# Kernel optimization log

Hardware: AMD Instinct MI355X
Metric: run time of the kernel (lower is better)

Reference implementation:

```python
import jax, jax.numpy as jnp
import numpy as np

N_NODES = 50000


def gcn_conv(x, src, dst, W, b, n_nodes):
    """PyG GCNConv: add self-loops, sym-normalize, aggregate, linear.
    x' = D^{-1/2} (A + I) D^{-1/2} X W + b
    """
    loop = jnp.arange(n_nodes, dtype=src.dtype)
    s = jnp.concatenate([src, loop])  # [E + N]
    d = jnp.concatenate([dst, loop])
    h = x @ W  # [N, out]
    deg = jax.ops.segment_sum(jnp.ones_like(d, dtype=h.dtype), d, num_segments=n_nodes)
    dinv = jnp.where(deg > 0, jax.lax.rsqrt(deg), 0.0)
    norm = dinv[s] * dinv[d]  # [E + N]
    msg = h[s] * norm[:, None]  # gather + scale (edge-level, memory bound)
    out = jax.ops.segment_sum(msg, d, num_segments=n_nodes)
    return out + b


def setup_inputs() -> dict:
    key = jax.random.key(0)
    k1, k2, k3, k4 = jax.random.split(key, 4)
    n, e, d_in, d_hid, d_out = N_NODES, 800000, 128, 128, 64
    x = jax.random.normal(k1, (n, d_in), dtype=jnp.float32)
    edge_index = jax.random.randint(k2, (2, e), 0, n, dtype=jnp.int64)
    W1 = jax.random.normal(k3, (d_in, d_hid), dtype=jnp.float32) * (1.0 / np.sqrt(d_in))
    b1 = jnp.zeros((d_hid,), dtype=jnp.float32)
    W2 = jax.random.normal(k4, (d_hid, d_out), dtype=jnp.float32) * (1.0 / np.sqrt(d_hid))
    b2 = jnp.zeros((d_out,), dtype=jnp.float32)
    return {"x": x, "edge_index": edge_index, "W1": W1, "b1": b1, "W2": W2, "b2": b2}


def reference(x, edge_index, W1, b1, W2, b2):
    src, dst = edge_index[0], edge_index[1]
    h = gcn_conv(x, src, dst, W1, b1, N_NODES)
    h = jax.nn.relu(h)
    h = gcn_conv(h, src, dst, W2, b2, N_NODES)
    # edge-wise gather + dot product -> per-edge logits [E]
    logits = jnp.sum(h[src] * h[dst], axis=-1)
    return logits
```

## Files before the change

### kernel.cpp

```cpp
#include <hip/hip_runtime.h>
#include <hip/hip_bf16.h>


__global__ void cnt_rank_k(const int* __restrict__ dst, int* __restrict__ cnt,
                           int* __restrict__ rank, int E) {
    int t = blockIdx.x * blockDim.x + threadIdx.x;
    int e = t * 4;
    if (e + 4 <= E) {
        int4 d4 = *reinterpret_cast<const int4*>(dst + e);
        int4 r4;
        r4.x = atomicAdd(&cnt[d4.x], 1);
        r4.y = atomicAdd(&cnt[d4.y], 1);
        r4.z = atomicAdd(&cnt[d4.z], 1);
        r4.w = atomicAdd(&cnt[d4.w], 1);
        *reinterpret_cast<int4*>(rank + e) = r4;
    } else {
        for (int i = e; i < E; i++) rank[i] = atomicAdd(&cnt[dst[i]], 1);
    }
}

__global__ void scan1_k(const int* __restrict__ cnt, int* __restrict__ incl,
                        int* __restrict__ bsum, int N) {
    __shared__ int sh[256];
    int i = blockIdx.x * 256 + threadIdx.x;
    int v = (i < N) ? cnt[i] : 0;
    sh[threadIdx.x] = v;
    __syncthreads();
#pragma unroll
    for (int off = 1; off < 256; off <<= 1) {
        int t = (threadIdx.x >= off) ? sh[threadIdx.x - off] : 0;
        __syncthreads();
        sh[threadIdx.x] += t;
        __syncthreads();
    }
    if (i < N) incl[i] = sh[threadIdx.x];
    if (threadIdx.x == 255) bsum[blockIdx.x] = sh[255];
}

__global__ __launch_bounds__(256) void scan23_k(const int* __restrict__ cnt,
                                                const int* __restrict__ incl,
                                                const int* __restrict__ bsum,
                                                int* __restrict__ rowptr,
                                                float* __restrict__ dinv,
                                                int N, int E, int NB) {
    __shared__ int sh[256];
    __shared__ int blockOff;
    int v = (threadIdx.x < NB) ? bsum[threadIdx.x] : 0;
    sh[threadIdx.x] = v;
    __syncthreads();
#pragma unroll
    for (int off = 1; off < 256; off <<= 1) {
        int t = (threadIdx.x >= off) ? sh[threadIdx.x - off] : 0;
        __syncthreads();
        sh[threadIdx.x] += t;
        __syncthreads();
    }
    if (threadIdx.x == blockIdx.x) blockOff = sh[threadIdx.x] - v;
    __syncthreads();
    int i = blockIdx.x * 256 + threadIdx.x;
    if (i < N) {
        int c = cnt[i];
        rowptr[i] = incl[i] - c + blockOff;
        dinv[i] = rsqrtf(1.0f + (float)c);
    }
    if (i == 0) rowptr[N] = E;
}

template <int BN, bool RELU>
__device__ __forceinline__ void gemm_body32(const float* __restrict__ A,
                                            const float* __restrict__ W,
                                            const float* __restrict__ dscale,
                                            float4* __restrict__ OutT,
                                            int M, int Nn, int row0,
                                            float (*As)[36], float (*Bs)[BN]) {
    constexpr int K = 128, BK = 16;
    constexpr int TN = BN / 16;
    const int tid = threadIdx.x;
    const int tx = tid & 15, ty = tid >> 4;

    float acc[2][TN];
#pragma unroll
    for (int m = 0; m < 2; m++)
#pragma unroll
        for (int n = 0; n < TN; n++) acc[m][n] = 0.0f;

    for (int kt = 0; kt < K; kt += BK) {
        if (tid < 128) {
            int r = tid >> 2;
            int kq = (tid & 3) * 4;
            float4 av = make_float4(0.f, 0.f, 0.f, 0.f);
            int gr = row0 + r;
            if (gr < M)
                av = *reinterpret_cast<const float4*>(A + (size_t)gr * K + kt + kq);
            if (RELU) {
                av.x = fmaxf(av.x, 0.f); av.y = fmaxf(av.y, 0.f);
                av.z = fmaxf(av.z, 0.f); av.w = fmaxf(av.w, 0.f);
            }
            As[kq + 0][r] = av.x; As[kq + 1][r] = av.y;
            As[kq + 2][r] = av.z; As[kq + 3][r] = av.w;
        }
#pragma unroll
        for (int s = 0; s < (BK * BN) / (256 * 4); s++) {
            int f = s * 256 + tid;
            int brow = f / (BN / 4);
            int bcol = (f % (BN / 4)) * 4;
            float4 bv = *reinterpret_cast<const float4*>(W + (size_t)(kt + brow) * BN + bcol);
            *reinterpret_cast<float4*>(&Bs[brow][bcol]) = bv;
        }
        __syncthreads();

#pragma unroll
        for (int k = 0; k < BK; k++) {
            float2 a2 = *reinterpret_cast<const float2*>(&As[k][ty * 2]);
            float a[2] = {a2.x, a2.y};
            float b[TN];
            float4 b0 = *reinterpret_cast<const float4*>(&Bs[k][tx * 4]);
            b[0] = b0.x; b[1] = b0.y; b[2] = b0.z; b[3] = b0.w;
            if (TN == 8) {
                float4 b1 = *reinterpret_cast<const float4*>(&Bs[k][64 + tx * 4]);
                b[4] = b1.x; b[5] = b1.y; b[6] = b1.z; b[7] = b1.w;
            }
#pragma unroll
            for (int m = 0; m < 2; m++)
#pragma unroll
                for (int n = 0; n < TN; n++) acc[m][n] = fmaf(a[m], b[n], acc[m][n]);
        }
        __syncthreads();
    }

    const int chunk0 = tx >> 2;
    const int off = tx & 3;
#pragma unroll
    for (int m = 0; m < 2; m++) {
        int gr = row0 + ty * 2 + m;
        if (gr < M) {
            float dv = dscale[gr];
            float4 o0 = make_float4(acc[m][0] * dv, acc[m][1] * dv,
                                    acc[m][2] * dv, acc[m][3] * dv);
            OutT[((size_t)chunk0 * Nn + gr) * 4 + off] = o0;
            if (TN == 8) {
                float4 o1 = make_float4(acc[m][4] * dv, acc[m][5] * dv,
                                        acc[m][6] * dv, acc[m][7] * dv);
                OutT[((size_t)(4 + chunk0) * Nn + gr) * 4 + off] = o1;
            }
        }
    }
}

__global__ __launch_bounds__(256) void gemm1_fill_k(const float* __restrict__ A,
                                                    const float* __restrict__ W,
                                                    const float* __restrict__ dscale,
                                                    float4* __restrict__ OutT,
                                                    int M, int Nn,
                                                    const int* __restrict__ src,
                                                    const int* __restrict__ dst,
                                                    const int* __restrict__ rowptr,
                                                    const int* __restrict__ rank,
                                                    int* __restrict__ col,
                                                    int* __restrict__ eid, int E,
                                                    int gemmBlocks) {
    __shared__ float As[16][36];
    __shared__ float Bs[16][128];
    int g = (int)blockIdx.x;
    if (g >= gemmBlocks) {
        int t = (g - gemmBlocks) * 256 + threadIdx.x;
        int e = t * 4;
        if (e + 4 <= E) {
            int4 s4 = *reinterpret_cast<const int4*>(src + e);
            int4 d4 = *reinterpret_cast<const int4*>(dst + e);
            int4 r4 = *reinterpret_cast<const int4*>(rank + e);
            int p0 = rowptr[d4.x] + r4.x; col[p0] = s4.x; eid[p0] = e + 0;
            int p1 = rowptr[d4.y] + r4.y; col[p1] = s4.y; eid[p1] = e + 1;
            int p2 = rowptr[d4.z] + r4.z; col[p2] = s4.z; eid[p2] = e + 2;
            int p3 = rowptr[d4.w] + r4.w; col[p3] = s4.w; eid[p3] = e + 3;
        } else {
            for (int i = e; i < E; i++) {
                int pos = rowptr[dst[i]] + rank[i];
                col[pos] = src[i]; eid[pos] = i;
            }
        }
        return;
    }
    gemm_body32<128, false>(A, W, dscale, OutT, M, Nn, g * 32, As, Bs);
}

__global__ __launch_bounds__(256) void gemm2_k(const float* __restrict__ A,
                                               const float* __restrict__ W,
                                               const float* __restrict__ dscale,
                                               float4* __restrict__ OutT,
                                               int M, int Nn) {
    __shared__ float As[16][36];
    __shared__ float Bs[16][64];
    gemm_body32<64, true>(A, W, dscale, OutT, M, Nn, (int)blockIdx.x * 32, As, Bs);
}

__global__ __launch_bounds__(256) void pull128c_k(const int* __restrict__ rowptr,
                                                  const int* __restrict__ col,
                                                  const float4* __restrict__ hsT,
                                                  const float* __restrict__ dinv,
                                                  const float4* __restrict__ bias4,
                                                  float4* __restrict__ out4, int N) {
    int c = (int)(blockIdx.x & 7);
    int g = (int)(blockIdx.x >> 3);
    int v = g * 64 + (int)(threadIdx.x >> 2);
    if (v >= N) return;
    int j = threadIdx.x & 3;
    int p0 = rowptr[v], p1 = rowptr[v + 1];
    size_t cb = (size_t)c * N;

    float4 acc = hsT[(cb + v) * 4 + j];
    int p = p0;
    for (; p + 4 <= p1; p += 4) {
        int u0 = col[p], u1 = col[p + 1], u2 = col[p + 2], u3 = col[p + 3];
        float4 a = hsT[(cb + u0) * 4 + j];
        float4 b = hsT[(cb + u1) * 4 + j];
        float4 cc = hsT[(cb + u2) * 4 + j];
        float4 d = hsT[(cb + u3) * 4 + j];
        acc.x += (a.x + b.x) + (cc.x + d.x);
        acc.y += (a.y + b.y) + (cc.y + d.y);
        acc.z += (a.z + b.z) + (cc.z + d.z);
        acc.w += (a.w + b.w) + (cc.w + d.w);
    }
    for (; p < p1; p++) {
        float4 a = hsT[(cb + col[p]) * 4 + j];
        acc.x += a.x; acc.y += a.y; acc.z += a.z; acc.w += a.w;
    }

    float dv = dinv[v];
    float4 bv = bias4[c * 4 + j];
    out4[(size_t)v * 32 + c * 4 + j] =
        make_float4(fmaf(acc.x, dv, bv.x), fmaf(acc.y, dv, bv.y),
                    fmaf(acc.z, dv, bv.z), fmaf(acc.w, dv, bv.w));
}

__global__ __launch_bounds__(256) void pull64c_k(const int* __restrict__ rowptr,
                                                 const int* __restrict__ col,
                                                 const float4* __restrict__ g2T,
                                                 const float* __restrict__ dinv,
                                                 const float4* __restrict__ bias4,
                                                 float4* __restrict__ out4, int N) {
    int c = (int)(blockIdx.x & 3);
    int g = (int)(blockIdx.x >> 2);
    int v = g * 64 + (int)(threadIdx.x >> 2);
    if (v >= N) return;
    int j = threadIdx.x & 3;
    int p0 = rowptr[v], p1 = rowptr[v + 1];
    size_t cb = (size_t)c * N;

    float4 acc = g2T[(cb + v) * 4 + j];
    int p = p0;
    for (; p + 4 <= p1; p += 4) {
        int u0 = col[p], u1 = col[p + 1], u2 = col[p + 2], u3 = col[p + 3];
        float4 a = g2T[(cb + u0) * 4 + j];
        float4 b = g2T[(cb + u1) * 4 + j];
        float4 cc = g2T[(cb + u2) * 4 + j];
        float4 d = g2T[(cb + u3) * 4 + j];
        acc.x += (a.x + b.x) + (cc.x + d.x);
        acc.y += (a.y + b.y) + (cc.y + d.y);
        acc.z += (a.z + b.z) + (cc.z + d.z);
        acc.w += (a.w + b.w) + (cc.w + d.w);
    }
    for (; p < p1; p++) {
        float4 a = g2T[(cb + col[p]) * 4 + j];
        acc.x += a.x; acc.y += a.y; acc.z += a.z; acc.w += a.w;
    }

    float dv = dinv[v];
    float4 bv = bias4[c * 4 + j];
    out4[(size_t)v * 16 + c * 4 + j] =
        make_float4(fmaf(acc.x, dv, bv.x), fmaf(acc.y, dv, bv.y),
                    fmaf(acc.z, dv, bv.z), fmaf(acc.w, dv, bv.w));
}

__global__ __launch_bounds__(256) void logits_csr_k(const int* __restrict__ rowptr,
                                                    const int* __restrict__ col,
                                                    const int* __restrict__ eid,
                                                    const float4* __restrict__ h4,
                                                    float* __restrict__ out, int N) {
    int v = (int)((blockIdx.x * (size_t)blockDim.x + threadIdx.x) >> 6);
    if (v >= N) return;
    int lane = threadIdx.x & 63;
    int q = lane & 15, slot = lane >> 4;
    int p0 = rowptr[v], p1 = rowptr[v + 1];
    if (p0 == p1) return;

    float4 rd = h4[(size_t)v * 16 + q];

    int p = p0;
    for (; p + 8 <= p1; p += 8) {
        int s0 = col[p + slot], s1 = col[p + 4 + slot];
        int e0 = eid[p + slot], e1 = eid[p + 4 + slot];
        float4 ra = h4[(size_t)s0 * 16 + q];
        float4 rb = h4[(size_t)s1 * 16 + q];
        float t0 = rd.x * ra.x + rd.y * ra.y + rd.z * ra.z + rd.w * ra.w;
        float t1 = rd.x * rb.x + rd.y * rb.y + rd.z * rb.z + rd.w * rb.w;
#pragma unroll
        for (int off = 1; off < 16; off <<= 1) {
            t0 += __shfl_xor(t0, off);
            t1 += __shfl_xor(t1, off);
        }
        if (q == 0) { out[e0] = t0; out[e1] = t1; }
    }
    for (; p + 4 <= p1; p += 4) {
        int s0 = col[p + slot];
        int e0 = eid[p + slot];
        float4 ra = h4[(size_t)s0 * 16 + q];
        float t0 = rd.x * ra.x + rd.y * ra.y + rd.z * ra.z + rd.w * ra.w;
#pragma unroll
        for (int off = 1; off < 16; off <<= 1) t0 += __shfl_xor(t0, off);
        if (q == 0) out[e0] = t0;
    }
    int rem = p1 - p;
    if (slot < rem) {
        int s0 = col[p + slot];
        int e0 = eid[p + slot];
        float4 ra = h4[(size_t)s0 * 16 + q];
        float t0 = rd.x * ra.x + rd.y * ra.y + rd.z * ra.z + rd.w * ra.w;
#pragma unroll
        for (int off = 1; off < 16; off <<= 1) t0 += __shfl_xor(t0, off);
        if (q == 0) out[e0] = t0;
    }
}

extern "C" void kernel_launch(void* const* d_in, const int* in_sizes, int n_in,
                              void* d_out, int out_size, void* d_ws, size_t ws_size,
                              hipStream_t stream) {
    const float* x  = (const float*)d_in[0];
    const int* ei   = (const int*)d_in[1];
    const float* W1 = (const float*)d_in[2];
    const float* b1 = (const float*)d_in[3];
    const float* W2 = (const float*)d_in[4];
    const float* b2 = (const float*)d_in[5];
    float* out = (float*)d_out;

    const int N = in_sizes[0] / 128;
    const int E = in_sizes[1] / 2;
    const int* src = ei;
    const int* dst = ei + E;

    float* ws   = (float*)d_ws;
    float* dinv = ws;
    float* bufA = ws + 50176;
    float* bufB = bufA + (size_t)N * 128;
    float* hsT  = bufA;
    float* agg1 = bufB;
    float* g2T  = bufA;
    float* agg2 = bufA + (size_t)N * 64;

    int* ibase  = (int*)(bufB + (size_t)N * 128);
    int* cnt    = ibase;
    int* incl   = cnt + N;
    int* rowptr = incl + N;
    int* bsum   = rowptr + (N + 1);
    int* rank   = bsum + 256;
    int* col    = rank + E;
    int* eid    = col + E;

    const int B = 256;
    const int NB = (N + 255) / 256;
    const unsigned nodeBlocks = (unsigned)(((size_t)N * 64 + 255) / 256);
    const unsigned ng64 = (unsigned)((N + 63) / 64);

    hipMemsetAsync(cnt, 0, (size_t)N * sizeof(int), stream);
    cnt_rank_k<<<(E / 4 + B - 1) / B, B, 0, stream>>>(dst, cnt, rank, E);
    scan1_k<<<NB, 256, 0, stream>>>(cnt, incl, bsum, N);
    scan23_k<<<NB, 256, 0, stream>>>(cnt, incl, bsum, rowptr, dinv, N, E, NB);

    {
        int gemmBlocks = (N + 31) / 32;
        int fillBlocks = (E / 4 + B - 1) / B;
        gemm1_fill_k<<<gemmBlocks + fillBlocks, 256, 0, stream>>>(
            x, W1, dinv, (float4*)hsT, N, N, src, dst, rowptr, rank, col, eid, E,
            gemmBlocks);
    }

    pull128c_k<<<ng64 * 8, 256, 0, stream>>>(rowptr, col, (const float4*)hsT, dinv,
                                             (const float4*)b1, (float4*)agg1, N);

    gemm2_k<<<(N + 31) / 32, 256, 0, stream>>>(agg1, W2, dinv, (float4*)g2T, N, N);

    pull64c_k<<<ng64 * 4, 256, 0, stream>>>(rowptr, col, (const float4*)g2T, dinv,
                                            (const float4*)b2, (float4*)agg2, N);

    logits_csr_k<<<nodeBlocks, 256, 0, stream>>>(rowptr, col, eid, (const float4*)agg2, out, N);
}
```

Baseline: 232.0 us.

## Compute edge logits in edge order from chunked layout with partial-sum reduction

Drops the eid permutation array and the CSR-ordered logits kernel. The second aggregation now writes its output in the chunk-transposed layout. Logits are computed directly in edge order: each of four column chunks writes a partial dot product per edge, and a second kernel sums the four partials with coalesced float4 loads. This removes the eid scatter writes and the scattered output stores, at the cost of an extra kernel, a 4×E partial buffer, and reading src and dst rows without the CSR locality.

```diff
diff --git a/kernel.cpp b/kernel.cpp
--- a/kernel.cpp
+++ b/kernel.cpp
@@ -156,8 +156,7 @@
                                                     const int* __restrict__ dst,
                                                     const int* __restrict__ rowptr,
                                                     const int* __restrict__ rank,
-                                                    int* __restrict__ col,
-                                                    int* __restrict__ eid, int E,
+                                                    int* __restrict__ col, int E,
                                                     int gemmBlocks) {
     __shared__ float As[16][36];
     __shared__ float Bs[16][128];
@@ -169,15 +168,13 @@
             int4 s4 = *reinterpret_cast<const int4*>(src + e);
             int4 d4 = *reinterpret_cast<const int4*>(dst + e);
             int4 r4 = *reinterpret_cast<const int4*>(rank + e);
-            int p0 = rowptr[d4.x] + r4.x; col[p0] = s4.x; eid[p0] = e + 0;
-            int p1 = rowptr[d4.y] + r4.y; col[p1] = s4.y; eid[p1] = e + 1;
-            int p2 = rowptr[d4.z] + r4.z; col[p2] = s4.z; eid[p2] = e + 2;
-            int p3 = rowptr[d4.w] + r4.w; col[p3] = s4.w; eid[p3] = e + 3;
+            col[rowptr[d4.x] + r4.x] = s4.x;
+            col[rowptr[d4.y] + r4.y] = s4.y;
+            col[rowptr[d4.z] + r4.z] = s4.z;
+            col[rowptr[d4.w] + r4.w] = s4.w;
         } else {
-            for (int i = e; i < E; i++) {
-                int pos = rowptr[dst[i]] + rank[i];
-                col[pos] = src[i]; eid[pos] = i;
-            }
+            for (int i = e; i < E; i++)
+                col[rowptr[dst[i]] + rank[i]] = src[i];
         }
         return;
     }
@@ -238,7 +235,7 @@
                                                  const float4* __restrict__ g2T,
                                                  const float* __restrict__ dinv,
                                                  const float4* __restrict__ bias4,
-                                                 float4* __restrict__ out4, int N) {
+                                                 float4* __restrict__ outT, int N) {
     int c = (int)(blockIdx.x & 3);
     int g = (int)(blockIdx.x >> 2);
     int v = g * 64 + (int)(threadIdx.x >> 2);
@@ -267,58 +264,58 @@
 
     float dv = dinv[v];
     float4 bv = bias4[c * 4 + j];
-    out4[(size_t)v * 16 + c * 4 + j] =
+    outT[(cb + v) * 4 + j] =
         make_float4(fmaf(acc.x, dv, bv.x), fmaf(acc.y, dv, bv.y),
                     fmaf(acc.z, dv, bv.z), fmaf(acc.w, dv, bv.w));
 }
 
-__global__ __launch_bounds__(256) void logits_csr_k(const int* __restrict__ rowptr,
-                                                    const int* __restrict__ col,
-                                                    const int* __restrict__ eid,
-                                                    const float4* __restrict__ h4,
-                                                    float* __restrict__ out, int N) {
-    int v = (int)((blockIdx.x * (size_t)blockDim.x + threadIdx.x) >> 6);
-    if (v >= N) return;
-    int lane = threadIdx.x & 63;
-    int q = lane & 15, slot = lane >> 4;
-    int p0 = rowptr[v], p1 = rowptr[v + 1];
-    if (p0 == p1) return;
-
-    float4 rd = h4[(size_t)v * 16 + q];
-
-    int p = p0;
-    for (; p + 8 <= p1; p += 8) {
-        int s0 = col[p + slot], s1 = col[p + 4 + slot];
-        int e0 = eid[p + slot], e1 = eid[p + 4 + slot];
-        float4 ra = h4[(size_t)s0 * 16 + q];
-        float4 rb = h4[(size_t)s1 * 16 + q];
-        float t0 = rd.x * ra.x + rd.y * ra.y + rd.z * ra.z + rd.w * ra.w;
-        float t1 = rd.x * rb.x + rd.y * rb.y + rd.z * rb.z + rd.w * rb.w;
-#pragma unroll
-        for (int off = 1; off < 16; off <<= 1) {
-            t0 += __shfl_xor(t0, off);
-            t1 += __shfl_xor(t1, off);
-        }
-        if (q == 0) { out[e0] = t0; out[e1] = t1; }
-    }
-    for (; p + 4 <= p1; p += 4) {
-        int s0 = col[p + slot];
-        int e0 = eid[p + slot];
-        float4 ra = h4[(size_t)s0 * 16 + q];
-        float t0 = rd.x * ra.x + rd.y * ra.y + rd.z * ra.z + rd.w * ra.w;
-#pragma unroll
-        for (int off = 1; off < 16; off <<= 1) t0 += __shfl_xor(t0, off);
-        if (q == 0) out[e0] = t0;
-    }
-    int rem = p1 - p;
-    if (slot < rem) {
-        int s0 = col[p + slot];
-        int e0 = eid[p + slot];
-        float4 ra = h4[(size_t)s0 * 16 + q];
-        float t0 = rd.x * ra.x + rd.y * ra.y + rd.z * ra.z + rd.w * ra.w;
-#pragma unroll
-        for (int off = 1; off < 16; off <<= 1) t0 += __shfl_xor(t0, off);
-        if (q == 0) out[e0] = t0;
+__global__ __launch_bounds__(256) void logits_part_k(const int* __restrict__ src,
+                                                     const int* __restrict__ dst,
+                                                     const float4* __restrict__ aggT,
+                                                     float* __restrict__ part,
+                                                     int N, int E) {
+    int c = (int)(blockIdx.x & 3);
+    int blk = (int)(blockIdx.x >> 2);
+    int g = (int)(threadIdx.x >> 2);
+    int j = threadIdx.x & 3;
+    size_t cb = (size_t)c * N;
+    int ebase = blk * 256;
+
+#pragma unroll
+    for (int i = 0; i < 4; i++) {
+        int e = ebase + i * 64 + g;
+        if (e < E) {
+            int s = src[e], d = dst[e];
+            float4 a = aggT[(cb + s) * 4 + j];
+            float4 b = aggT[(cb + d) * 4 + j];
+            float t = a.x * b.x + a.y * b.y + a.z * b.z + a.w * b.w;
+            t += __shfl_xor(t, 1);
+            t += __shfl_xor(t, 2);
+            if (j == 0) part[(size_t)c * E + e] = t;
+        }
+    }
+}
+
+__global__ __launch_bounds__(256) void logits_reduce_k(const float* __restrict__ part,
+                                                       float* __restrict__ out, int E) {
+    int i = blockIdx.x * blockDim.x + threadIdx.x;
+    int e4 = E >> 2;
+    if (i < e4) {
+        const float4* p0 = reinterpret_cast<const float4*>(part);
+        const float4* p1 = reinterpret_cast<const float4*>(part + (size_t)E);
+        const float4* p2 = reinterpret_cast<const float4*>(part + (size_t)E * 2);
+        const float4* p3 = reinterpret_cast<const float4*>(part + (size_t)E * 3);
+        float4 a = p0[i], b = p1[i], c = p2[i], d = p3[i];
+        float4 o = make_float4((a.x + b.x) + (c.x + d.x), (a.y + b.y) + (c.y + d.y),
+                               (a.z + b.z) + (c.z + d.z), (a.w + b.w) + (c.w + d.w));
+        reinterpret_cast<float4*>(out)[i] = o;
+    }
+    int tail = e4 * 4 + i;
+    if (i < (E & 3) + 0 && false) {}
+    if (blockIdx.x == 0 && threadIdx.x < (E & 3)) {
+        int e = e4 * 4 + threadIdx.x;
+        out[e] = part[e] + part[(size_t)E + e] + part[(size_t)E * 2 + e] +
+                 part[(size_t)E * 3 + e];
     }
 }
 
@@ -338,14 +335,15 @@
     const int* src = ei;
     const int* dst = ei + E;
 
-    float* ws   = (float*)d_ws;
-    float* dinv = ws;
-    float* bufA = ws + 50176;
-    float* bufB = bufA + (size_t)N * 128;
-    float* hsT  = bufA;
-    float* agg1 = bufB;
-    float* g2T  = bufA;
-    float* agg2 = bufA + (size_t)N * 64;
+    float* ws    = (float*)d_ws;
+    float* dinv  = ws;
+    float* bufA  = ws + 50176;
+    float* bufB  = bufA + (size_t)N * 128;
+    float* hsT   = bufA;
+    float* agg1  = bufB;
+    float* g2T   = bufA;
+    float* agg2T = bufA + (size_t)N * 64;
+    float* part  = bufB;
 
     int* ibase  = (int*)(bufB + (size_t)N * 128);
     int* cnt    = ibase;
@@ -354,11 +352,9 @@
     int* bsum   = rowptr + (N + 1);
     int* rank   = bsum + 256;
     int* col    = rank + E;
-    int* eid    = col + E;
 
     const int B = 256;
     const int NB = (N + 255) / 256;
-    const unsigned nodeBlocks = (unsigned)(((size_t)N * 64 + 255) / 256);
     const unsigned ng64 = (unsigned)((N + 63) / 64);
 
     hipMemsetAsync(cnt, 0, (size_t)N * sizeof(int), stream);
@@ -370,7 +366,7 @@
         int gemmBlocks = (N + 31) / 32;
         int fillBlocks = (E / 4 + B - 1) / B;
         gemm1_fill_k<<<gemmBlocks + fillBlocks, 256, 0, stream>>>(
-            x, W1, dinv, (float4*)hsT, N, N, src, dst, rowptr, rank, col, eid, E,
+            x, W1, dinv, (float4*)hsT, N, N, src, dst, rowptr, rank, col, E,
             gemmBlocks);
     }
 
@@ -380,7 +376,13 @@
     gemm2_k<<<(N + 31) / 32, 256, 0, stream>>>(agg1, W2, dinv, (float4*)g2T, N, N);
 
     pull64c_k<<<ng64 * 4, 256, 0, stream>>>(rowptr, col, (const float4*)g2T, dinv,
-                                            (const float4*)b2, (float4*)agg2, N);
-
-    logits_csr_k<<<nodeBlocks, 256, 0, stream>>>(rowptr, col, eid, (const float4*)agg2, out, N);
-}
+                                            (const float4*)b2, (float4*)agg2T, N);
+
+    {
+        unsigned blk = (unsigned)((E + 255) / 256);
+        logits_part_k<<<blk * 4, 256, 0, stream>>>(src, dst, (const float4*)agg2T,
+                                                   part, N, E);
+        unsigned rblk = (unsigned)((E / 4 + 255) / 256);
+        logits_reduce_k<<<rblk, 256, 0, stream>>>(part, out, E);
+    }
+}
```

Measured after the change: 224.8 us. 1.03x faster.
